# Kernel optimization log

Hardware: AMD Instinct MI355X
Metric: run time of the kernel (lower is better)

Reference implementation:

```python
import jax, jax.numpy as jnp
import numpy as np


def setup_inputs() -> dict:
    key = jax.random.key(0)
    k1, k2 = jax.random.split(key)
    B, T = 16, 2048
    n_fft = 1024
    hop_length = 256
    win_length = 1024
    N = n_fft // 2 + 1  # 513 rfft bins
    spec_real = jax.random.normal(k1, (B, N, T), dtype=jnp.float32)
    spec_imag = jax.random.normal(k2, (B, N, T), dtype=jnp.float32)
    # periodic Hann window (torch.hann_window default)
    n = jnp.arange(win_length, dtype=jnp.float32)
    window = 0.5 * (1.0 - jnp.cos(2.0 * jnp.pi * n / win_length))
    return {
        "spec_real": spec_real,
        "spec_imag": spec_imag,
        "window": window,
        "n_fft": n_fft,
        "hop_length": hop_length,
        "win_length": win_length,
    }


def reference(spec_real, spec_imag, window, n_fft, hop_length, win_length):
    pad = (win_length - hop_length) // 2
    B, N, T = spec_real.shape
    spec = spec_real + 1j * spec_imag  # [B, N, T] complex
    # irfft along freq dim with 'backward' norm (jnp default): [B, n_fft, T]
    ifft = jnp.fft.irfft(spec, n=n_fft, axis=1)
    ifft = ifft * window[None, :, None]  # windowed frames
    L = (T - 1) * hop_length + win_length  # overlap-add output length
    # scatter indices: sample positions of each frame, shape [win_length, T]
    idx = jnp.arange(T)[None, :] * hop_length + jnp.arange(win_length)[:, None]
    y = jnp.zeros((B, L), dtype=ifft.dtype).at[:, idx].add(ifft)
    y = y[:, pad:L - pad]
    # window-squared envelope, same overlap-add pattern
    wsq = jnp.broadcast_to((window * window)[:, None], (win_length, T))
    env = jnp.zeros((L,), dtype=window.dtype).at[idx].add(wsq)[pad:L - pad]
    return y / env
```

## Files before the change

kernel.cpp:

```cpp
#include <hip/hip_runtime.h>

#define BB 16
#define TT 2048
#define NFREQ 513
#define MHALF 512
#define HOP 256
#define WIN 1024
#define LPAD 525056
#define PAD 384
#define OUTL 524288
#define FT 8
#define OLA_LEN (FT*HOP + (WIN-HOP))

__device__ __forceinline__ int brev9(int k) {
  return (int)(__brev((unsigned)k) >> 23);
}

__global__ __launch_bounds__(256) void istft_frames(
    const float* __restrict__ sr, const float* __restrict__ si,
    float* __restrict__ y)
{
  __shared__ float zr[MHALF][FT + 1];
  __shared__ float zi[MHALF][FT + 1];
  __shared__ float ola[OLA_LEN];
  __shared__ float twc[256], tws[256];

  const int tid  = threadIdx.x;
  const int b    = blockIdx.x / (TT / FT);
  const int tile = blockIdx.x % (TT / FT);
  const int t0   = tile * FT;

  {
    float s, c;
    __sincosf((float)tid * 0.01227184630308513f, &s, &c);
    twc[tid] = c; tws[tid] = s;
  }
  for (int i = tid; i < OLA_LEN; i += 256) ola[i] = 0.f;

  const int f  = tid & (FT - 1);
  const int kg = tid >> 3;
  const float* srb = sr + (size_t)b * NFREQ * TT + t0 + f;
  const float* sib = si + (size_t)b * NFREQ * TT + t0 + f;

  for (int c = 0; c < 8; ++c) {
    int k = c * 32 + kg;
    float ar  = srb[(size_t)k * TT];
    float ai  = sib[(size_t)k * TT];
    float br_ = srb[(size_t)(MHALF - k) * TT];
    float bi_ = sib[(size_t)(MHALF - k) * TT];
    if (k == 0) {
      zr[0][f] = 0.5f * (ar + br_);
      zi[0][f] = 0.5f * (ar - br_);
      float cr = srb[(size_t)256 * TT];
      float ci = sib[(size_t)256 * TT];
      zr[1][f] = cr;
      zi[1][f] = -ci;
    } else {
      float st, ct;
      __sincosf((float)k * 0.006135923151542565f, &st, &ct);
      float Er = 0.5f * (ar + br_), Ei = 0.5f * (ai - bi_);
      float Dr = 0.5f * (ar - br_), Di = 0.5f * (ai + bi_);
      float Or = Dr * ct - Di * st,  Oi = Dr * st + Di * ct;
      int p  = brev9(k);
      zr[p][f]  = Er - Oi;
      zi[p][f]  = Ei + Or;
      int p2 = brev9(MHALF - k);
      zr[p2][f] = Er + Oi;
      zi[p2][f] = Or - Ei;
    }
  }

  const int pp = tid >> 3;
  for (int s = 0; s < 9; ++s) {
    __syncthreads();
    const int h = 1 << s;
    #pragma unroll
    for (int i = 0; i < 8; ++i) {
      int bf  = pp + 32 * i;
      int ilo = bf & (h - 1);
      int ihi = bf >> s;
      int i0  = ihi * (h << 1) + ilo;
      int i1  = i0 + h;
      int tj  = ilo << (8 - s);
      float wr = twc[tj], wi = tws[tj];
      float ur = zr[i0][f], ui = zi[i0][f];
      float vr = zr[i1][f], vi = zi[i1][f];
      float tr = vr * wr - vi * wi;
      float ti = vr * wi + vi * wr;
      zr[i0][f] = ur + tr; zi[i0][f] = ui + ti;
      zr[i1][f] = ur - tr; zi[i1][f] = ui - ti;
    }
  }

  for (int g = 0; g < 4; ++g) {
    __syncthreads();
    int fr = g + 4 * (tid >> 7);
    int mb = tid & 127;
    #pragma unroll
    for (int i = 0; i < 4; ++i) {
      int m = mb + 128 * i;
      float re = zr[m][fr] * (1.0f / 512.0f);
      float im = zi[m][fr] * (1.0f / 512.0f);
      int j0 = 2 * m;
      float w0 = 0.5f - 0.5f * __cosf((float)j0       * 0.006135923151542565f);
      float w1 = 0.5f - 0.5f * __cosf((float)(j0 + 1) * 0.006135923151542565f);
      ola[fr * HOP + j0]     += re * w0;
      ola[fr * HOP + j0 + 1] += im * w1;
    }
  }
  __syncthreads();

  size_t ybase = (size_t)b * LPAD + (size_t)t0 * HOP;
  for (int i = 0; i < OLA_LEN / 256; ++i) {
    int idx = tid + 256 * i;
    float v = ola[idx];
    if (idx < (WIN - HOP) || idx >= FT * HOP) atomicAdd(&y[ybase + idx], v);
    else                                      y[ybase + idx] = v;
  }
}

__global__ __launch_bounds__(256) void istft_finalize(
    const float* __restrict__ y, const float* __restrict__ w,
    float* __restrict__ out)
{
  int gid = blockIdx.x * 256 + threadIdx.x;
  int b   = gid >> 17;
  int oo  = (gid & 131071) << 2;
  const float* yp = y + (size_t)b * LPAD + PAD + oo;
  float4 v = *(const float4*)yp;
  float r[4] = {v.x, v.y, v.z, v.w};
  float o[4];
  int l0 = PAD + oo;
  if (l0 >= (WIN - HOP) && l0 + 3 <= (TT - 1) * HOP + HOP - 1) {
    #pragma unroll
    for (int i = 0; i < 4; ++i) o[i] = r[i] * (2.0f / 3.0f);
  } else {
    #pragma unroll
    for (int i = 0; i < 4; ++i) {
      int l  = l0 + i;
      int j0 = l & 255;
      int tb = l >> 8;
      float env = 0.f;
      #pragma unroll
      for (int m2 = 0; m2 < 4; ++m2) {
        int t = tb - m2;
        if (t >= 0 && t < TT) { float ww = w[j0 + 256 * m2]; env += ww * ww; }
      }
      o[i] = r[i] / env;
    }
  }
  float4 vo = make_float4(o[0], o[1], o[2], o[3]);
  *(float4*)(out + ((size_t)gid << 2)) = vo;
}

extern "C" void kernel_launch(void* const* d_in, const int* in_sizes, int n_in,
                              void* d_out, int out_size, void* d_ws, size_t ws_size,
                              hipStream_t stream) {
  const float* sr = (const float*)d_in[0];
  const float* si = (const float*)d_in[1];
  const float* w  = (const float*)d_in[2];
  float* y   = (float*)d_ws;
  float* out = (float*)d_out;

  hipMemsetAsync(d_ws, 0, (size_t)BB * LPAD * sizeof(float), stream);
  istft_frames<<<BB * (TT / FT), 256, 0, stream>>>(sr, si, y);
  istft_finalize<<<(BB * (OUTL / 4)) / 256, 256, 0, stream>>>(y, w, out);
}
```

Before: 260.3 us.

## Fuse iSTFT into one kernel with output-owned tiles and radix-4 FFT

Replaces the memset, the frame kernel with atomic overlap-add and the finalize kernel with one fused kernel. Each block owns a 28-hop output span and recomputes the two halo frames on each side, so overlap-add stays in shared memory and output is written once with the envelope applied. The FFT moves from radix-2 to radix-4 stages over an XOR-swizzled float2 shared buffer. This removes the global workspace round trip, the atomics and the extra launches, at the cost of redundant halo frame work (32 frames computed per 28 kept) and only 1184 blocks.

```diff
diff --git a/kernel.cpp b/kernel.cpp
--- a/kernel.cpp
+++ b/kernel.cpp
@@ -2,155 +2,160 @@
 
 #define BB 16
 #define TT 2048
-#define NFREQ 513
-#define MHALF 512
+#define NROW 513
 #define HOP 256
-#define WIN 1024
-#define LPAD 525056
-#define PAD 384
-#define OUTL 524288
-#define FT 8
-#define OLA_LEN (FT*HOP + (WIN-HOP))
+#define OUTLB 524288
+#define FTO 28
+#define SPAN (FTO*HOP)
+#define TILES 74
+#define NCH 4
+#define RZ 513
 
-__device__ __forceinline__ int brev9(int k) {
-  return (int)(__brev((unsigned)k) >> 23);
-}
+__device__ __forceinline__ int brev9(int k){ return (int)(__brev((unsigned)k)>>23); }
+__device__ __forceinline__ int zidx(int f,int m){ return f*RZ + (m ^ ((m>>4)&28) ^ (f<<2)); }
 
-__global__ __launch_bounds__(256) void istft_frames(
+__global__ __launch_bounds__(256,2) void istft_fused(
     const float* __restrict__ sr, const float* __restrict__ si,
-    float* __restrict__ y)
+    float* __restrict__ out)
 {
-  __shared__ float zr[MHALF][FT + 1];
-  __shared__ float zi[MHALF][FT + 1];
-  __shared__ float ola[OLA_LEN];
-  __shared__ float twc[256], tws[256];
+  __shared__ float2 zc[8*RZ];
+  __shared__ __align__(16) float2 ola[SPAN/2];
+  __shared__ float2 ttab[256];
 
   const int tid  = threadIdx.x;
-  const int b    = blockIdx.x / (TT / FT);
-  const int tile = blockIdx.x % (TT / FT);
-  const int t0   = tile * FT;
+  const int b    = blockIdx.x / TILES;
+  const int tile = blockIdx.x % TILES;
+  const int L0   = tile*SPAN + 384;
+  const int Tbase= tile*FTO - 2;
 
-  {
-    float s, c;
-    __sincosf((float)tid * 0.01227184630308513f, &s, &c);
-    twc[tid] = c; tws[tid] = s;
-  }
-  for (int i = tid; i < OLA_LEN; i += 256) ola[i] = 0.f;
+  { float s,c; __sincosf((float)tid*0.012271846303085130f,&s,&c); ttab[tid]=make_float2(c,s); }
+  for (int i=tid;i<SPAN/2;i+=256) ola[i]=make_float2(0.f,0.f);
 
-  const int f  = tid & (FT - 1);
-  const int kg = tid >> 3;
-  const float* srb = sr + (size_t)b * NFREQ * TT + t0 + f;
-  const float* sib = si + (size_t)b * NFREQ * TT + t0 + f;
+  const int f  = tid & 7;
+  const int pp = tid >> 3;
+  const float* srb = sr + (size_t)b*NROW*TT;
+  const float* sib = si + (size_t)b*NROW*TT;
 
-  for (int c = 0; c < 8; ++c) {
-    int k = c * 32 + kg;
-    float ar  = srb[(size_t)k * TT];
-    float ai  = sib[(size_t)k * TT];
-    float br_ = srb[(size_t)(MHALF - k) * TT];
-    float bi_ = sib[(size_t)(MHALF - k) * TT];
-    if (k == 0) {
-      zr[0][f] = 0.5f * (ar + br_);
-      zi[0][f] = 0.5f * (ar - br_);
-      float cr = srb[(size_t)256 * TT];
-      float ci = sib[(size_t)256 * TT];
-      zr[1][f] = cr;
-      zi[1][f] = -ci;
-    } else {
-      float st, ct;
-      __sincosf((float)k * 0.006135923151542565f, &st, &ct);
-      float Er = 0.5f * (ar + br_), Ei = 0.5f * (ai - bi_);
-      float Dr = 0.5f * (ar - br_), Di = 0.5f * (ai + bi_);
-      float Or = Dr * ct - Di * st,  Oi = Dr * st + Di * ct;
-      int p  = brev9(k);
-      zr[p][f]  = Er - Oi;
-      zi[p][f]  = Ei + Or;
-      int p2 = brev9(MHALF - k);
-      zr[p2][f] = Er + Oi;
-      zi[p2][f] = Or - Ei;
+  for (int c = 0; c < NCH; ++c) {
+    const int t  = Tbase + 8*c + f;
+    const int tc = min(max(t,0),TT-1);
+    const float msk = (t>=0 && t<TT) ? 1.f : 0.f;
+    __syncthreads();
+
+    for (int cc=0; cc<8; ++cc) {
+      int k = cc*32 + pp;
+      float ar = srb[(size_t)k*TT + tc]*msk;
+      float ai = sib[(size_t)k*TT + tc]*msk;
+      float br = srb[(size_t)(512-k)*TT + tc]*msk;
+      float bi = sib[(size_t)(512-k)*TT + tc]*msk;
+      if (k==0) {
+        zc[zidx(f,0)] = make_float2(0.5f*(ar+br), 0.5f*(ar-br));
+        float cr = srb[(size_t)256*TT + tc]*msk;
+        float ci = sib[(size_t)256*TT + tc]*msk;
+        zc[zidx(f,1)] = make_float2(cr,-ci);
+      } else {
+        float st,ct; __sincosf((float)k*0.006135923151542565f,&st,&ct);
+        float Er=0.5f*(ar+br), Ei=0.5f*(ai-bi);
+        float Dr=0.5f*(ar-br), Di=0.5f*(ai+bi);
+        float Or=Dr*ct-Di*st,  Oi=Dr*st+Di*ct;
+        zc[zidx(f,brev9(k))]     = make_float2(Er-Oi, Ei+Or);
+        zc[zidx(f,brev9(512-k))] = make_float2(Er+Oi, Or-Ei);
+      }
     }
-  }
 
-  const int pp = tid >> 3;
-  for (int s = 0; s < 9; ++s) {
+    for (int st=0; st<4; ++st) {
+      __syncthreads();
+      const int h = 1<<(2*st);
+      #pragma unroll
+      for (int i=0;i<4;++i) {
+        int q   = pp + 32*i;
+        int ilo = q & (h-1);
+        int base= ((q>>(2*st))<<(2*st+2)) + ilo;
+        float2 w1 = ttab[ilo<<(8-2*st)];
+        float2 w2 = ttab[ilo<<(7-2*st)];
+        float2 e0=zc[zidx(f,base)],     e1=zc[zidx(f,base+h)];
+        float2 e2=zc[zidx(f,base+2*h)], e3=zc[zidx(f,base+3*h)];
+        float t1r=e1.x*w1.x-e1.y*w1.y, t1i=e1.x*w1.y+e1.y*w1.x;
+        float t3r=e3.x*w1.x-e3.y*w1.y, t3i=e3.x*w1.y+e3.y*w1.x;
+        float arr=e0.x+t1r, ari=e0.y+t1i, brr=e0.x-t1r, bri=e0.y-t1i;
+        float crr=e2.x+t3r, cri=e2.y+t3i, drr=e2.x-t3r, dri=e2.y-t3i;
+        float cwr=crr*w2.x-cri*w2.y, cwi=crr*w2.y+cri*w2.x;
+        float dwr=drr*w2.x-dri*w2.y, dwi=drr*w2.y+dri*w2.x;
+        zc[zidx(f,base)]     = make_float2(arr+cwr, ari+cwi);
+        zc[zidx(f,base+2*h)] = make_float2(arr-cwr, ari-cwi);
+        zc[zidx(f,base+h)]   = make_float2(brr-dwi, bri+dwr);
+        zc[zidx(f,base+3*h)] = make_float2(brr+dwi, bri-dwr);
+      }
+    }
     __syncthreads();
-    const int h = 1 << s;
     #pragma unroll
-    for (int i = 0; i < 8; ++i) {
-      int bf  = pp + 32 * i;
-      int ilo = bf & (h - 1);
-      int ihi = bf >> s;
-      int i0  = ihi * (h << 1) + ilo;
-      int i1  = i0 + h;
-      int tj  = ilo << (8 - s);
-      float wr = twc[tj], wi = tws[tj];
-      float ur = zr[i0][f], ui = zi[i0][f];
-      float vr = zr[i1][f], vi = zi[i1][f];
-      float tr = vr * wr - vi * wi;
-      float ti = vr * wi + vi * wr;
-      zr[i0][f] = ur + tr; zi[i0][f] = ui + ti;
-      zr[i1][f] = ur - tr; zi[i1][f] = ui - ti;
+    for (int i=0;i<8;++i) {
+      int q = pp + 32*i;
+      float2 tw = ttab[q];
+      float2 u = zc[zidx(f,q)], v = zc[zidx(f,q+256)];
+      float tr=v.x*tw.x-v.y*tw.y, ti=v.x*tw.y+v.y*tw.x;
+      zc[zidx(f,q)]     = make_float2(u.x+tr, u.y+ti);
+      zc[zidx(f,q+256)] = make_float2(u.x-tr, u.y-ti);
     }
-  }
 
-  for (int g = 0; g < 4; ++g) {
-    __syncthreads();
-    int fr = g + 4 * (tid >> 7);
-    int mb = tid & 127;
-    #pragma unroll
-    for (int i = 0; i < 4; ++i) {
-      int m = mb + 128 * i;
-      float re = zr[m][fr] * (1.0f / 512.0f);
-      float im = zi[m][fr] * (1.0f / 512.0f);
-      int j0 = 2 * m;
-      float w0 = 0.5f - 0.5f * __cosf((float)j0       * 0.006135923151542565f);
-      float w1 = 0.5f - 0.5f * __cosf((float)(j0 + 1) * 0.006135923151542565f);
-      ola[fr * HOP + j0]     += re * w0;
-      ola[fr * HOP + j0 + 1] += im * w1;
+    for (int g=0; g<4; ++g) {
+      __syncthreads();
+      int slot = g + 4*(tid>>7);
+      int tg   = Tbase + 8*c + slot;
+      int offB = tg*HOP - L0;
+      bool vt  = (tg>=0 && tg<TT);
+      int mb   = tid & 127;
+      #pragma unroll
+      for (int i=0;i<4;++i) {
+        int m = mb + 128*i;
+        float2 v = zc[zidx(slot,m)];
+        int j0 = 2*m;
+        float w0 = 0.5f-0.5f*__cosf((float)j0    *0.006135923151542565f);
+        float w1v= 0.5f-0.5f*__cosf((float)(j0+1)*0.006135923151542565f);
+        int idx = offB + j0;
+        if (vt && idx>=0 && idx<SPAN) {
+          float2 o = ola[idx>>1];
+          o.x += v.x*(1.f/512.f)*w0;
+          o.y += v.y*(1.f/512.f)*w1v;
+          ola[idx>>1] = o;
+        }
+      }
     }
   }
   __syncthreads();
 
-  size_t ybase = (size_t)b * LPAD + (size_t)t0 * HOP;
-  for (int i = 0; i < OLA_LEN / 256; ++i) {
-    int idx = tid + 256 * i;
-    float v = ola[idx];
-    if (idx < (WIN - HOP) || idx >= FT * HOP) atomicAdd(&y[ybase + idx], v);
-    else                                      y[ybase + idx] = v;
-  }
-}
-
-__global__ __launch_bounds__(256) void istft_finalize(
-    const float* __restrict__ y, const float* __restrict__ w,
-    float* __restrict__ out)
-{
-  int gid = blockIdx.x * 256 + threadIdx.x;
-  int b   = gid >> 17;
-  int oo  = (gid & 131071) << 2;
-  const float* yp = y + (size_t)b * LPAD + PAD + oo;
-  float4 v = *(const float4*)yp;
-  float r[4] = {v.x, v.y, v.z, v.w};
-  float o[4];
-  int l0 = PAD + oo;
-  if (l0 >= (WIN - HOP) && l0 + 3 <= (TT - 1) * HOP + HOP - 1) {
-    #pragma unroll
-    for (int i = 0; i < 4; ++i) o[i] = r[i] * (2.0f / 3.0f);
-  } else {
-    #pragma unroll
-    for (int i = 0; i < 4; ++i) {
-      int l  = l0 + i;
-      int j0 = l & 255;
-      int tb = l >> 8;
-      float env = 0.f;
-      #pragma unroll
-      for (int m2 = 0; m2 < 4; ++m2) {
-        int t = tb - m2;
-        if (t >= 0 && t < TT) { float ww = w[j0 + 256 * m2]; env += ww * ww; }
+  const bool edge = (tile==0)|(tile==TILES-1);
+  float* outb = out + (size_t)b*OUTLB;
+  for (int i=0;i<7;++i) {
+    int i4 = tid + 256*i;
+    int s  = 4*i4;
+    int gs = tile*SPAN + s;
+    if (gs < OUTLB) {
+      float4 v = ((const float4*)ola)[i4];
+      float r[4]={v.x,v.y,v.z,v.w};
+      if (!edge) {
+        #pragma unroll
+        for(int e=0;e<4;++e) r[e] *= (2.f/3.f);
+      } else {
+        #pragma unroll
+        for(int e=0;e<4;++e) {
+          int l = L0 + s + e;
+          int j0 = l & 255, tb = l >> 8;
+          float env=0.f;
+          #pragma unroll
+          for (int mm=0;mm<4;++mm) {
+            int t2 = tb-mm;
+            if (t2>=0 && t2<TT) {
+              float wv = 0.5f-0.5f*__cosf((float)(j0+256*mm)*0.006135923151542565f);
+              env += wv*wv;
+            }
+          }
+          r[e] /= env;
+        }
       }
-      o[i] = r[i] / env;
+      *(float4*)(outb+gs) = make_float4(r[0],r[1],r[2],r[3]);
     }
   }
-  float4 vo = make_float4(o[0], o[1], o[2], o[3]);
-  *(float4*)(out + ((size_t)gid << 2)) = vo;
 }
 
 extern "C" void kernel_launch(void* const* d_in, const int* in_sizes, int n_in,
@@ -158,11 +163,6 @@
                               hipStream_t stream) {
   const float* sr = (const float*)d_in[0];
   const float* si = (const float*)d_in[1];
-  const float* w  = (const float*)d_in[2];
-  float* y   = (float*)d_ws;
   float* out = (float*)d_out;
-
-  hipMemsetAsync(d_ws, 0, (size_t)BB * LPAD * sizeof(float), stream);
-  istft_frames<<<BB * (TT / FT), 256, 0, stream>>>(sr, si, y);
-  istft_finalize<<<(BB * (OUTL / 4)) / 256, 256, 0, stream>>>(y, w, out);
+  istft_fused<<<BB*TILES, 256, 0, stream>>>(sr, si, out);
 }
```

New measurement: 260.1 us. Within noise of the previous version (-0.1%).
